# Optimization experiments

Measured on AMD Instinct MI355X. Metric: run time of the kernel, lower is better.

The kernel has to match this reference:

```python
import jax, jax.numpy as jnp
import numpy as np

BN_EPS = 1e-5


def conv3x3(x, w):
    # 3x3 'same' conv, stride 1, no bias (matches nn.Conv2d(k=3, padding=1, bias=False))
    return jax.lax.conv_general_dilated(
        x, w, window_strides=(1, 1), padding='SAME',
        dimension_numbers=('NCHW', 'OIHW', 'NCHW'))


def batchnorm(x, gamma, beta, mean, var):
    # eval-mode BatchNorm2d with running stats
    scale = (gamma / jnp.sqrt(var + BN_EPS))[None, :, None, None]
    return (x - mean[None, :, None, None]) * scale + beta[None, :, None, None]


def setup_inputs() -> dict:
    key = jax.random.key(0)
    ks = jax.random.split(key, 13)
    B, C, H, W = 16, 64, 160, 160
    wshape = (C, C, 3, 3)
    inp = {
        'x': jax.random.normal(ks[0], (B, C, H, W), jnp.float32),
        'w_cv1': jax.random.normal(ks[1], wshape, jnp.float32) * 0.05,
        'g1': jax.random.uniform(ks[2], (C,), jnp.float32, 0.5, 1.5),
        'b1': jax.random.normal(ks[3], (C,), jnp.float32) * 0.1,
        'm1': jax.random.normal(ks[4], (C,), jnp.float32) * 0.1,
        'v1': jax.random.uniform(ks[5], (C,), jnp.float32, 0.5, 1.5),
        'wq': jax.random.normal(ks[6], wshape, jnp.float32) * 0.05,
        'wk': jax.random.normal(ks[7], wshape, jnp.float32) * 0.05,
        'wv': jax.random.normal(ks[8], wshape, jnp.float32) * 0.05,
        'g2': jax.random.uniform(ks[9], (C,), jnp.float32, 0.5, 1.5),
        'b2': jax.random.normal(ks[10], (C,), jnp.float32) * 0.1,
        'm2': jax.random.normal(ks[11], (C,), jnp.float32) * 0.1,
        'v2': jax.random.uniform(ks[12], (C,), jnp.float32, 0.5, 1.5),
    }
    return inp


def reference(x, w_cv1, g1, b1, m1, v1, wq, wk, wv, g2, b2, m2, v2):
    # cv1: Conv -> BN -> SiLU
    y = jax.nn.silu(batchnorm(conv3x3(x, w_cv1), g1, b1, m1, v1))

    # CSA_ConvBlock on y (c_ channels)
    fq = conv3x3(y, wq)   # [B,C,H,W]
    fk = conv3x3(y, wk)
    fv = conv3x3(y, wv)
    H, W = y.shape[2], y.shape[3]

    # Original: f_sim[b,i,j,h1,h2] = sum_w fq[b,i,h1,w]*fk[b,j,h2,w] / sqrt(W);
    # then sum over j, then mean-ish sum over (h1,h2)/H^2 -> f_scores[b,i].
    # Algebraically identical reorder (sum-before-matmul):
    k_sum = fk.sum(axis=(1, 2))                       # [B,W], sum over channels j and rows h2
    scale = 1.0 / (float(W) ** 0.5 * float(H) * float(H))
    f_scores = jnp.einsum('bchw,bw->bc', fq, k_sum) * scale  # [B,C]
    scores = jax.nn.softmax(f_scores, axis=1)[:, :, None, None]

    r = scores * fv + y
    r = jax.nn.relu(batchnorm(r, g2, b2, m2, v2))

    # shortcut: c1 == c2 and shortcut=True
    return x + r
```

## Files before the change

kernel.cpp:

```cpp
#include <hip/hip_runtime.h>
#include <hip/hip_bf16.h>
#include <math.h>

#define NB 16
#define NC 64
#define NH 160
#define NW 160

typedef __attribute__((ext_vector_type(8))) short bf16x8;
typedef __attribute__((ext_vector_type(4))) float f32x4;
typedef __attribute__((ext_vector_type(8))) unsigned short u16x8;
typedef __attribute__((ext_vector_type(4))) unsigned short u16x4;

__device__ __forceinline__ unsigned short f2bf(float v) {
  union { __hip_bfloat16 b; unsigned short u; } cv; cv.b = __float2bfloat16(v); return cv.u;
}
__device__ __forceinline__ float bf2f(unsigned short u) {
  union { unsigned u; float f; } cv; cv.u = ((unsigned)u) << 16; return cv.f;
}

__global__ void pack_w_kernel3(const float* __restrict__ wA, const float* __restrict__ wB,
                               const float* __restrict__ wq, const float* __restrict__ wk,
                               unsigned short* __restrict__ apkA, unsigned short* __restrict__ apkB,
                               float* __restrict__ wqt, float* __restrict__ wkst) {
  int idx = blockIdx.x * 256 + threadIdx.x;
  if (idx < 2 * 36864) {
    const float* w = (idx < 36864) ? wA : wB;
    unsigned short* apk = (idx < 36864) ? apkA : apkB;
    int i = (idx < 36864) ? idx : idx - 36864;
    int j = i & 7, l = (i >> 3) & 63, rest = i >> 9;
    int ks = rest % 18, ct = rest / 18;
    int cih = ks & 1, tap = ks >> 1, kh = tap / 3, kw = tap % 3;
    int co = ct * 16 + (l & 15), ci = cih * 32 + (l >> 4) * 8 + j;
    apk[i] = f2bf(w[(((size_t)co * NC + ci) * 3 + kh) * 3 + kw]);
  } else if (idx < 3 * 36864) {
    int i2 = idx - 2 * 36864;
    int c = i2 & 63, tau = i2 >> 6;
    int i = tau & 63, jj = tau >> 6;
    wqt[i2] = wq[(size_t)c * 576 + i * 9 + jj];
  } else if (idx < 3 * 36864 + 576) {
    int i3 = idx - 3 * 36864;
    int i = i3 & 63, jj = i3 >> 6;
    float s = 0.f;
    for (int cj = 0; cj < NC; ++cj) s += wk[(size_t)cj * 576 + i * 9 + jj];
    wkst[i3] = s;
  }
}

__global__ __launch_bounds__(256) void to_nhwc(const float* __restrict__ x,
                                               unsigned short* __restrict__ xt) {
  __shared__ unsigned short l[64 * 162];
  int bh = blockIdx.x; int b = bh / NH, h = bh % NH;
  for (int i = threadIdx.x; i < 64 * NW; i += 256) {
    int ci = i / NW, w = i % NW;
    l[ci * 162 + w] = f2bf(x[(((size_t)b * NC + ci) * NH + h) * NW + w]);
  }
  __syncthreads();
  unsigned short* o = xt + ((size_t)b * NH + h) * NW * NC;
  for (int i = threadIdx.x; i < NW * 8; i += 256) {
    int w = i >> 3, s = i & 7;
    u16x8 v;
#pragma unroll
    for (int j = 0; j < 8; ++j) v[j] = l[(s * 8 + j) * 162 + w];
    *(u16x8*)&o[w * 64 + s * 8] = v;
  }
}

template<bool FINAL>
__global__ __launch_bounds__(256, FINAL ? 3 : 2) void conv3x3_mfma6(
    const unsigned short* __restrict__ in_nhwc, const unsigned short* __restrict__ apk,
    const float* __restrict__ gg, const float* __restrict__ bbeta,
    const float* __restrict__ mmean, const float* __restrict__ vvar,
    void* __restrict__ outv, const float* __restrict__ scores,
    const float* __restrict__ xres, float* __restrict__ colpart)
{
  __shared__ unsigned short ring[6 * 34 * 64];
  __shared__ unsigned short epi[FINAL ? 8 : 2 * 32 * 72];
  __shared__ f32x4 csv[FINAL ? 1 : 512];

  const int t = threadIdx.x, lane = t & 63, wave = t >> 6;
  const int q = lane >> 4, col = lane & 15;

  int g = blockIdx.x;
  int sw = (g & 7) * 160 + (g >> 3);
  const int b = sw / 80;
  int rem = sw % 80;
  const int h0 = (rem / 5) * 10, w0 = (rem % 5) * 32;

  float scR[4], shR[4], scoR[4];
#pragma unroll
  for (int r = 0; r < 4; ++r) {
    int co = wave * 16 + q * 4 + r;
    float s = gg[co] * rsqrtf(vvar[co] + 1e-5f);
    scR[r] = s; shR[r] = bbeta[co] - mmean[co] * s;
    scoR[r] = FINAL ? scores[b * NC + co] : 0.f;
  }

  bf16x8 wf[18];
#pragma unroll
  for (int ks = 0; ks < 18; ++ks)
    wf[ks] = *(const bf16x8*)&apk[((size_t)(wave * 18 + ks) * 64 + lane) * 8];

  const unsigned short* inb = in_nhwc + (size_t)b * NH * NW * 64;

#define SLOT(R) ((int)((unsigned)((R) + 1) % 6u) * 2176)
#define STG_ISSUE(ROW, V0, V1, A0, A1)                                        \
  { int row_ = (ROW);                                                         \
    bool rowok_ = (unsigned)row_ < (unsigned)NH;                              \
    int slot_ = SLOT(row_);                                                   \
    { int wcc = t >> 3, s8 = t & 7; int wsrc = w0 + wcc - 1;                  \
      A0 = slot_ + wcc * 64 + ((s8 ^ (wcc & 7)) << 3);                        \
      V0 = (u16x8){};                                                         \
      if (rowok_ && (unsigned)wsrc < (unsigned)NW)                            \
        V0 = *(const u16x8*)&inb[((size_t)row_ * NW + wsrc) * 64 + s8 * 8];   \
    }                                                                         \
    if (t < 16) { int c = 256 + t; int wcc = c >> 3, s8 = c & 7;              \
      int wsrc = w0 + wcc - 1;                                                \
      A1 = slot_ + wcc * 64 + ((s8 ^ (wcc & 7)) << 3);                        \
      V1 = (u16x8){};                                                         \
      if (rowok_ && (unsigned)wsrc < (unsigned)NW)                            \
        V1 = *(const u16x8*)&inb[((size_t)row_ * NW + wsrc) * 64 + s8 * 8];   \
    } }
#define STG_COMMIT(V0, V1, A0, A1)                                            \
  *(u16x8*)&ring[A0] = V0;                                                    \
  if (t < 16) *(u16x8*)&ring[A1] = V1;

  if constexpr (!FINAL) {
    csv[t] = (f32x4){0.f, 0.f, 0.f, 0.f};
    csv[t + 256] = (f32x4){0.f, 0.f, 0.f, 0.f};
  }
  for (int rr = -1; rr <= 2; ++rr) {
    u16x8 v0, v1 = {}; int a0, a1 = 0;
    STG_ISSUE(h0 + rr, v0, v1, a0, a1)
    STG_COMMIT(v0, v1, a0, a1)
  }
  __syncthreads();

  for (int wi = 0; wi < 5; ++wi) {
    const int h = h0 + wi * 2;
    u16x8 va0, va1 = {}, vb0, vb1 = {}; int aa0, aa1 = 0, ab0, ab1 = 0;
    const bool doS = (wi < 4);
    if (doS) {
      STG_ISSUE(h + 3, va0, va1, aa0, aa1)
      STG_ISSUE(h + 4, vb0, vb1, ab0, ab1)
    }

    const int sl[4] = { SLOT(h - 1), SLOT(h), SLOT(h + 1), SLOT(h + 2) };
    f32x4 acc[2][2];
#pragma unroll
    for (int o = 0; o < 2; ++o) { acc[o][0] = (f32x4){0,0,0,0}; acc[o][1] = (f32x4){0,0,0,0}; }

#pragma unroll
    for (int ri = 0; ri < 4; ++ri) {
#pragma unroll
      for (int kw = 0; kw < 3; ++kw) {
#pragma unroll
        for (int cih = 0; cih < 2; ++cih) {
          const int wcb = col + kw;
          const int ea = sl[ri] + wcb * 64 + (((cih << 2) + q) ^ (wcb & 7)) * 8;
          const bf16x8* bp = (const bf16x8*)&ring[ea];
          bf16x8 B0 = bp[0], B1 = bp[128];
          if (ri <= 2) {
            const int ks = (ri * 3 + kw) * 2 + cih;
            acc[0][0] = __builtin_amdgcn_mfma_f32_16x16x32_bf16(wf[ks], B0, acc[0][0], 0, 0, 0);
            acc[0][1] = __builtin_amdgcn_mfma_f32_16x16x32_bf16(wf[ks], B1, acc[0][1], 0, 0, 0);
          }
          if (ri >= 1) {
            const int ks = ((ri - 1) * 3 + kw) * 2 + cih;
            acc[1][0] = __builtin_amdgcn_mfma_f32_16x16x32_bf16(wf[ks], B0, acc[1][0], 0, 0, 0);
            acc[1][1] = __builtin_amdgcn_mfma_f32_16x16x32_bf16(wf[ks], B1, acc[1][1], 0, 0, 0);
          }
        }
      }
    }

    if constexpr (!FINAL) {
      f32x4 csadd[2];
      csadd[0] = (f32x4){0,0,0,0}; csadd[1] = (f32x4){0,0,0,0};
#pragma unroll
      for (int o = 0; o < 2; ++o) {
#pragma unroll
        for (int wt = 0; wt < 2; ++wt) {
          u16x4 ev;
#pragma unroll
          for (int r = 0; r < 4; ++r) {
            float z = scR[r] * acc[o][wt][r] + shR[r];
            ev[r] = f2bf(z / (1.f + __expf(-z)));
          }
          *(u16x4*)&epi[((o * 32) + wt * 16 + col) * 72 + wave * 16 + q * 4] = ev;
#pragma unroll
          for (int r = 0; r < 4; ++r) csadd[wt][r] += bf2f(ev[r]);
        }
      }
      { int cc = wave * 4 + q;
        csv[cc * 32 + col]      += csadd[0];
        csv[cc * 32 + 16 + col] += csadd[1]; }
      if (doS) { STG_COMMIT(va0, va1, aa0, aa1) STG_COMMIT(vb0, vb1, ab0, ab1) }
      __syncthreads();
      { int w = t >> 3, s = t & 7;
#pragma unroll
        for (int o = 0; o < 2; ++o) {
          unsigned short* yo = (unsigned short*)outv + (((size_t)b * NH + h + o) * NW + w0) * 64;
          *(u16x8*)&yo[w * 64 + s * 8] = *(const u16x8*)&epi[((o * 32) + w) * 72 + s * 8];
        }
      }
      __syncthreads();
    } else {
      if (doS) { STG_COMMIT(va0, va1, aa0, aa1) STG_COMMIT(vb0, vb1, ab0, ab1) }
      float* outp = (float*)outv;
#pragma unroll
      for (int o = 0; o < 2; ++o) {
        const int rb1 = sl[1 + o];
#pragma unroll
        for (int wt = 0; wt < 2; ++wt) {
          int wcc = wt * 16 + col + 1;
          int gr = (wave * 2 + (q >> 1)) ^ (wcc & 7);
          u16x4 yv = *(const u16x4*)&ring[rb1 + wcc * 64 + gr * 8 + (q & 1) * 4];
#pragma unroll
          for (int r = 0; r < 4; ++r) {
            int co = wave * 16 + q * 4 + r;
            float rv = scoR[r] * acc[o][wt][r] + bf2f(yv[r]);
            float rb_ = scR[r] * rv + shR[r];
            rb_ = fmaxf(rb_, 0.f);
            size_t oi = (((size_t)b * NC + co) * NH + h + o) * NW + w0 + wt * 16 + col;
            outp[oi] = xres[oi] + rb_;
          }
        }
      }
      __syncthreads();
    }
  }

  if constexpr (!FINAL) {
    const int strip = h0 / 10;
    float* pp = colpart + (((size_t)b * 16 + strip) * NW + w0) * 64;
    int w = t >> 3, g0 = t & 7;
    *(f32x4*)&pp[w * 64 + g0 * 4]       = csv[g0 * 32 + w];
    *(f32x4*)&pp[w * 64 + (g0 + 8) * 4] = csv[(g0 + 8) * 32 + w];
  }
#undef STG_ISSUE
#undef STG_COMMIT
#undef SLOT
}

__global__ void colsum2_kernel(const float* __restrict__ part, float* __restrict__ ycol) {
  int id = blockIdx.x * 256 + threadIdx.x;
  if (id >= NB * NW * NC) return;
  int c = id & 63; int bw = id >> 6; int w = bw % NW; int b = bw / NW;
  const float* p = part + (((size_t)b * 16) * NW + w) * 64 + c;
  float s = 0.f;
#pragma unroll
  for (int st = 0; st < 16; ++st) s += p[(size_t)st * NW * 64];
  ycol[id] = s;
}

__device__ __forceinline__ float zval(const float* __restrict__ ycol,
                                      const unsigned short* __restrict__ y,
                                      int b, int i, int kh, int wp) {
  float z = ycol[((size_t)b * NW + wp) * 64 + i];
  if (kh == 0) z -= bf2f(y[(((size_t)b * NH + (NH - 1)) * NW + wp) * 64 + i]);
  if (kh == 2) z -= bf2f(y[(((size_t)b * NH) * NW + wp) * 64 + i]);
  return z;
}

__global__ __launch_bounds__(256) void ks_kernel(
    const float* __restrict__ ycol, const unsigned short* __restrict__ y,
    const float* __restrict__ wkst, float* __restrict__ ks)
{
  int id = blockIdx.x * 4 + (threadIdx.x >> 6);
  int lane = threadIdx.x & 63;
  int b = id / NW, w = id % NW;
  float s = 0.f;
#pragma unroll
  for (int jj = 0; jj < 9; ++jj) {
    int kh = jj / 3, kw = jj % 3;
    int wp = w + kw - 1;
    if ((unsigned)wp < (unsigned)NW)
      s += wkst[jj * 64 + lane] * zval(ycol, y, b, lane, kh, wp);
  }
#pragma unroll
  for (int off = 32; off; off >>= 1) s += __shfl_xor(s, off);
  if (lane == 0) ks[id] = s;
}

__global__ __launch_bounds__(256) void u_kernel(
    const float* __restrict__ ycol, const unsigned short* __restrict__ y,
    const float* __restrict__ ks, float* __restrict__ U)
{
  __shared__ float red[4][64];
  int bid = blockIdx.x;
  int b = bid / 9, jj = bid % 9;
  int kh = jj / 3, kw = jj % 3;
  int i = threadIdx.x & 63, ch = threadIdx.x >> 6;
  float s = 0.f;
  for (int w = ch * 40; w < ch * 40 + 40; ++w) {
    int wp = w + kw - 1;
    if ((unsigned)wp < (unsigned)NW)
      s += zval(ycol, y, b, i, kh, wp) * ks[b * NW + w];
  }
  red[ch][i] = s;
  __syncthreads();
  if (threadIdx.x < 64)
    U[((size_t)b * 9 + jj) * 64 + threadIdx.x] =
        red[0][threadIdx.x] + red[1][threadIdx.x] + red[2][threadIdx.x] + red[3][threadIdx.x];
}

__global__ __launch_bounds__(256) void scores_kernel2(
    const float* __restrict__ wqt, const float* __restrict__ U,
    float* __restrict__ scores)
{
  __shared__ float red[4][64];
  int b = blockIdx.x;
  int c = threadIdx.x & 63, p = threadIdx.x >> 6;
  const float* Ub = U + (size_t)b * 576;
  float s = 0.f;
  for (int tau = p * 144; tau < p * 144 + 144; ++tau)
    s += wqt[(size_t)tau * 64 + c] * Ub[tau];
  red[p][c] = s;
  __syncthreads();
  if (threadIdx.x < 64) {
    const float scale = 1.0f / (sqrtf((float)NW) * (float)NH * (float)NH);
    float f = (red[0][c] + red[1][c] + red[2][c] + red[3][c]) * scale;
    float mx = f;
#pragma unroll
    for (int off = 32; off; off >>= 1) mx = fmaxf(mx, __shfl_xor(mx, off));
    float e = __expf(f - mx);
    float sm = e;
#pragma unroll
    for (int off = 32; off; off >>= 1) sm += __shfl_xor(sm, off);
    scores[b * NC + c] = e / sm;
  }
}

extern "C" void kernel_launch(void* const* d_in, const int* in_sizes, int n_in,
                              void* d_out, int out_size, void* d_ws, size_t ws_size,
                              hipStream_t stream) {
  const float* x  = (const float*)d_in[0];
  const float* w1 = (const float*)d_in[1];
  const float* g1 = (const float*)d_in[2];
  const float* b1 = (const float*)d_in[3];
  const float* m1 = (const float*)d_in[4];
  const float* v1 = (const float*)d_in[5];
  const float* wq = (const float*)d_in[6];
  const float* wk = (const float*)d_in[7];
  const float* wv = (const float*)d_in[8];
  const float* g2 = (const float*)d_in[9];
  const float* b2 = (const float*)d_in[10];
  const float* m2 = (const float*)d_in[11];
  const float* v2 = (const float*)d_in[12];
  float* out = (float*)d_out;

  unsigned short* apk1 = (unsigned short*)d_ws;
  unsigned short* apk2 = apk1 + 36864;
  float* wqt  = (float*)(apk2 + 36864);
  float* wkst = wqt + 36864;
  float* ycol = wkst + 576;
  float* ks   = ycol + NB * NW * NC;
  float* U    = ks + NB * NW;
  float* scr  = U + NB * 576;
  float* part = scr + 1024;
  unsigned short* xt = (unsigned short*)(part + (size_t)NB * 16 * NW * 64);
  unsigned short* y  = xt + (size_t)NB * NH * NW * 64;

  pack_w_kernel3<<<dim3(435), 256, 0, stream>>>(w1, wv, wq, wk, apk1, apk2, wqt, wkst);
  to_nhwc<<<dim3(NB * NH), 256, 0, stream>>>(x, xt);

  conv3x3_mfma6<false><<<dim3(1280), 256, 0, stream>>>(
      xt, apk1, g1, b1, m1, v1, (void*)y, nullptr, nullptr, part);

  colsum2_kernel<<<dim3((NB * NW * NC + 255) / 256), 256, 0, stream>>>(part, ycol);
  ks_kernel<<<dim3(NB * NW / 4), 256, 0, stream>>>(ycol, y, wkst, ks);
  u_kernel<<<dim3(NB * 9), 256, 0, stream>>>(ycol, y, ks, U);
  scores_kernel2<<<dim3(NB), 256, 0, stream>>>(wqt, U, scr);

  conv3x3_mfma6<true><<<dim3(1280), 256, 0, stream>>>(
      y, apk2, g2, b2, m2, v2, (void*)out, scr, x, nullptr);
}
```

Measured before the change: 183.7 us.

## Fuse NCHW-to-NHWC bf16 conversion into first conv and double-buffer epilogue

Drops the separate to_nhwc kernel: the first conv now reads fp32 NCHW input directly, converts it to bf16 and writes the swizzled ring buffer in shared memory. This avoids a full write and re-read of a bf16 NHWC copy of x. The epilogue staging buffer is double-buffered so one barrier per step can be removed, and barriers become a lgkmcnt wait plus s_barrier. The final conv's launch bound drops from 3 to 2 waves per SIMD. The trade-off is strided fp32 channel loads (8 scalar loads per thread across channel planes) in place of 16-byte vector loads, plus more shared memory.

After: 150.4 us (median of 4 runs). -18.2%, faster.

```diff
diff --git a/kernel.cpp b/kernel.cpp
--- a/kernel.cpp
+++ b/kernel.cpp
@@ -18,6 +18,12 @@
 __device__ __forceinline__ float bf2f(unsigned short u) {
   union { unsigned u; float f; } cv; cv.u = ((unsigned)u) << 16; return cv.f;
 }
+
+#define LGKM_BARRIER()                                  \
+  asm volatile("s_waitcnt lgkmcnt(0)" ::: "memory");    \
+  __builtin_amdgcn_sched_barrier(0);                    \
+  __builtin_amdgcn_s_barrier();                         \
+  __builtin_amdgcn_sched_barrier(0);
 
 __global__ void pack_w_kernel3(const float* __restrict__ wA, const float* __restrict__ wB,
                                const float* __restrict__ wq, const float* __restrict__ wk,
@@ -47,35 +53,17 @@
   }
 }
 
-__global__ __launch_bounds__(256) void to_nhwc(const float* __restrict__ x,
-                                               unsigned short* __restrict__ xt) {
-  __shared__ unsigned short l[64 * 162];
-  int bh = blockIdx.x; int b = bh / NH, h = bh % NH;
-  for (int i = threadIdx.x; i < 64 * NW; i += 256) {
-    int ci = i / NW, w = i % NW;
-    l[ci * 162 + w] = f2bf(x[(((size_t)b * NC + ci) * NH + h) * NW + w]);
-  }
-  __syncthreads();
-  unsigned short* o = xt + ((size_t)b * NH + h) * NW * NC;
-  for (int i = threadIdx.x; i < NW * 8; i += 256) {
-    int w = i >> 3, s = i & 7;
-    u16x8 v;
-#pragma unroll
-    for (int j = 0; j < 8; ++j) v[j] = l[(s * 8 + j) * 162 + w];
-    *(u16x8*)&o[w * 64 + s * 8] = v;
-  }
-}
-
 template<bool FINAL>
-__global__ __launch_bounds__(256, FINAL ? 3 : 2) void conv3x3_mfma6(
-    const unsigned short* __restrict__ in_nhwc, const unsigned short* __restrict__ apk,
+__global__ __launch_bounds__(256, 2) void conv3x3_mfma7(
+    const unsigned short* __restrict__ in_nhwc, const float* __restrict__ in_nchw,
+    const unsigned short* __restrict__ apk,
     const float* __restrict__ gg, const float* __restrict__ bbeta,
     const float* __restrict__ mmean, const float* __restrict__ vvar,
     void* __restrict__ outv, const float* __restrict__ scores,
     const float* __restrict__ xres, float* __restrict__ colpart)
 {
   __shared__ unsigned short ring[6 * 34 * 64];
-  __shared__ unsigned short epi[FINAL ? 8 : 2 * 32 * 72];
+  __shared__ unsigned short epi[FINAL ? 8 : 2 * 64 * 72];
   __shared__ f32x4 csv[FINAL ? 1 : 512];
 
   const int t = threadIdx.x, lane = t & 63, wave = t >> 6;
@@ -101,10 +89,12 @@
   for (int ks = 0; ks < 18; ++ks)
     wf[ks] = *(const bf16x8*)&apk[((size_t)(wave * 18 + ks) * 64 + lane) * 8];
 
-  const unsigned short* inb = in_nhwc + (size_t)b * NH * NW * 64;
+  const unsigned short* inb = FINAL ? in_nhwc + (size_t)b * NH * NW * 64 : nullptr;
+  const float* xb = FINAL ? nullptr : in_nchw + (size_t)b * NC * NH * NW;
 
 #define SLOT(R) ((int)((unsigned)((R) + 1) % 6u) * 2176)
-#define STG_ISSUE(ROW, V0, V1, A0, A1)                                        \
+
+#define STGF_ISSUE(ROW, V0, V1, A0, A1)                                       \
   { int row_ = (ROW);                                                         \
     bool rowok_ = (unsigned)row_ < (unsigned)NH;                              \
     int slot_ = SLOT(row_);                                                   \
@@ -121,28 +111,78 @@
       if (rowok_ && (unsigned)wsrc < (unsigned)NW)                            \
         V1 = *(const u16x8*)&inb[((size_t)row_ * NW + wsrc) * 64 + s8 * 8];   \
     } }
-#define STG_COMMIT(V0, V1, A0, A1)                                            \
+#define STGF_COMMIT(V0, V1, A0, A1)                                           \
   *(u16x8*)&ring[A0] = V0;                                                    \
   if (t < 16) *(u16x8*)&ring[A1] = V1;
+
+#define STG1_ISSUE(ROW, F0, F1, A0, A1)                                       \
+  { int row_ = (ROW);                                                         \
+    bool rowok_ = (unsigned)row_ < (unsigned)NH;                              \
+    int slot_ = SLOT(row_);                                                   \
+    { int wcc = t % 34, s8 = t / 34; int wsrc = w0 + wcc - 1;                 \
+      A0 = slot_ + wcc * 64 + ((s8 ^ (wcc & 7)) << 3);                        \
+      bool ok_ = rowok_ && (unsigned)wsrc < (unsigned)NW;                     \
+      if (ok_) {                                                              \
+        const float* xp_ = xb + ((size_t)(s8 * 8) * NH + row_) * NW + wsrc;   \
+        _Pragma("unroll") for (int j_ = 0; j_ < 8; ++j_)                      \
+          F0[j_] = xp_[(size_t)j_ * NH * NW];                                 \
+      } else {                                                                \
+        _Pragma("unroll") for (int j_ = 0; j_ < 8; ++j_) F0[j_] = 0.f;        \
+      }                                                                       \
+    }                                                                         \
+    if (t < 16) { int wcc = 18 + t; int wsrc = w0 + wcc - 1;                  \
+      A1 = slot_ + wcc * 64 + ((7 ^ (wcc & 7)) << 3);                         \
+      bool ok_ = rowok_ && (unsigned)wsrc < (unsigned)NW;                     \
+      if (ok_) {                                                              \
+        const float* xp_ = xb + ((size_t)56 * NH + row_) * NW + wsrc;         \
+        _Pragma("unroll") for (int j_ = 0; j_ < 8; ++j_)                      \
+          F1[j_] = xp_[(size_t)j_ * NH * NW];                                 \
+      } else {                                                                \
+        _Pragma("unroll") for (int j_ = 0; j_ < 8; ++j_) F1[j_] = 0.f;        \
+      }                                                                       \
+    } }
+#define STG1_COMMIT(F0, F1, A0, A1)                                           \
+  { u16x8 pv_;                                                                \
+    _Pragma("unroll") for (int j_ = 0; j_ < 8; ++j_) pv_[j_] = f2bf(F0[j_]);  \
+    *(u16x8*)&ring[A0] = pv_; }                                               \
+  if (t < 16) { u16x8 pv_;                                                    \
+    _Pragma("unroll") for (int j_ = 0; j_ < 8; ++j_) pv_[j_] = f2bf(F1[j_]);  \
+    *(u16x8*)&ring[A1] = pv_; }
 
   if constexpr (!FINAL) {
     csv[t] = (f32x4){0.f, 0.f, 0.f, 0.f};
     csv[t + 256] = (f32x4){0.f, 0.f, 0.f, 0.f};
   }
-  for (int rr = -1; rr <= 2; ++rr) {
-    u16x8 v0, v1 = {}; int a0, a1 = 0;
-    STG_ISSUE(h0 + rr, v0, v1, a0, a1)
-    STG_COMMIT(v0, v1, a0, a1)
-  }
-  __syncthreads();
+
+  if constexpr (FINAL) {
+    for (int rr = -1; rr <= 2; ++rr) {
+      u16x8 v0, v1 = {}; int a0, a1 = 0;
+      STGF_ISSUE(h0 + rr, v0, v1, a0, a1)
+      STGF_COMMIT(v0, v1, a0, a1)
+    }
+  } else {
+    for (int rr = -1; rr <= 2; ++rr) {
+      float f0[8], f1[8]; int a0, a1 = 0;
+      STG1_ISSUE(h0 + rr, f0, f1, a0, a1)
+      STG1_COMMIT(f0, f1, a0, a1)
+    }
+  }
+  LGKM_BARRIER()
 
   for (int wi = 0; wi < 5; ++wi) {
     const int h = h0 + wi * 2;
+    const bool doS = (wi < 4);
+
     u16x8 va0, va1 = {}, vb0, vb1 = {}; int aa0, aa1 = 0, ab0, ab1 = 0;
-    const bool doS = (wi < 4);
+    float fa0[8], fa1[8], fb0[8], fb1[8];
     if (doS) {
-      STG_ISSUE(h + 3, va0, va1, aa0, aa1)
-      STG_ISSUE(h + 4, vb0, vb1, ab0, ab1)
+      if constexpr (FINAL) {
+        STGF_ISSUE(h + 3, va0, va1, aa0, aa1)
+        STGF_ISSUE(h + 4, vb0, vb1, ab0, ab1)
+      } else {
+        STG1_ISSUE(h + 3, fa0, fa1, aa0, aa1)
+        STG1_ISSUE(h + 4, fb0, fb1, ab0, ab1)
+      }
     }
 
     const int sl[4] = { SLOT(h - 1), SLOT(h), SLOT(h + 1), SLOT(h + 2) };
@@ -175,6 +215,7 @@
     }
 
     if constexpr (!FINAL) {
+      const int buf = (wi & 1) * 4608;
       f32x4 csadd[2];
       csadd[0] = (f32x4){0,0,0,0}; csadd[1] = (f32x4){0,0,0,0};
 #pragma unroll
@@ -187,7 +228,7 @@
             float z = scR[r] * acc[o][wt][r] + shR[r];
             ev[r] = f2bf(z / (1.f + __expf(-z)));
           }
-          *(u16x4*)&epi[((o * 32) + wt * 16 + col) * 72 + wave * 16 + q * 4] = ev;
+          *(u16x4*)&epi[buf + ((o * 32) + wt * 16 + col) * 72 + wave * 16 + q * 4] = ev;
 #pragma unroll
           for (int r = 0; r < 4; ++r) csadd[wt][r] += bf2f(ev[r]);
         }
@@ -195,18 +236,17 @@
       { int cc = wave * 4 + q;
         csv[cc * 32 + col]      += csadd[0];
         csv[cc * 32 + 16 + col] += csadd[1]; }
-      if (doS) { STG_COMMIT(va0, va1, aa0, aa1) STG_COMMIT(vb0, vb1, ab0, ab1) }
-      __syncthreads();
+      if (doS) { STG1_COMMIT(fa0, fa1, aa0, aa1) STG1_COMMIT(fb0, fb1, ab0, ab1) }
+      LGKM_BARRIER()
       { int w = t >> 3, s = t & 7;
 #pragma unroll
         for (int o = 0; o < 2; ++o) {
           unsigned short* yo = (unsigned short*)outv + (((size_t)b * NH + h + o) * NW + w0) * 64;
-          *(u16x8*)&yo[w * 64 + s * 8] = *(const u16x8*)&epi[((o * 32) + w) * 72 + s * 8];
+          *(u16x8*)&yo[w * 64 + s * 8] = *(const u16x8*)&epi[buf + ((o * 32) + w) * 72 + s * 8];
         }
       }
-      __syncthreads();
     } else {
-      if (doS) { STG_COMMIT(va0, va1, aa0, aa1) STG_COMMIT(vb0, vb1, ab0, ab1) }
+      if (doS) { STGF_COMMIT(va0, va1, aa0, aa1) STGF_COMMIT(vb0, vb1, ab0, ab1) }
       float* outp = (float*)outv;
 #pragma unroll
       for (int o = 0; o < 2; ++o) {
@@ -227,7 +267,7 @@
           }
         }
       }
-      __syncthreads();
+      LGKM_BARRIER()
     }
   }
 
@@ -238,8 +278,10 @@
     *(f32x4*)&pp[w * 64 + g0 * 4]       = csv[g0 * 32 + w];
     *(f32x4*)&pp[w * 64 + (g0 + 8) * 4] = csv[(g0 + 8) * 32 + w];
   }
-#undef STG_ISSUE
-#undef STG_COMMIT
+#undef STG1_ISSUE
+#undef STG1_COMMIT
+#undef STGF_ISSUE
+#undef STGF_COMMIT
 #undef SLOT
 }
 
@@ -359,20 +401,18 @@
   float* U    = ks + NB * NW;
   float* scr  = U + NB * 576;
   float* part = scr + 1024;
-  unsigned short* xt = (unsigned short*)(part + (size_t)NB * 16 * NW * 64);
-  unsigned short* y  = xt + (size_t)NB * NH * NW * 64;
+  unsigned short* y = (unsigned short*)(part + (size_t)NB * 16 * NW * 64);
 
   pack_w_kernel3<<<dim3(435), 256, 0, stream>>>(w1, wv, wq, wk, apk1, apk2, wqt, wkst);
-  to_nhwc<<<dim3(NB * NH), 256, 0, stream>>>(x, xt);
-
-  conv3x3_mfma6<false><<<dim3(1280), 256, 0, stream>>>(
-      xt, apk1, g1, b1, m1, v1, (void*)y, nullptr, nullptr, part);
+
+  conv3x3_mfma7<false><<<dim3(1280), 256, 0, stream>>>(
+      nullptr, x, apk1, g1, b1, m1, v1, (void*)y, nullptr, nullptr, part);
 
   colsum2_kernel<<<dim3((NB * NW * NC + 255) / 256), 256, 0, stream>>>(part, ycol);
   ks_kernel<<<dim3(NB * NW / 4), 256, 0, stream>>>(ycol, y, wkst, ks);
   u_kernel<<<dim3(NB * 9), 256, 0, stream>>>(ycol, y, ks, U);
   scores_kernel2<<<dim3(NB), 256, 0, stream>>>(wqt, U, scr);
 
-  conv3x3_mfma6<true><<<dim3(1280), 256, 0, stream>>>(
-      y, apk2, g2, b2, m2, v2, (void*)out, scr, x, nullptr);
-}
+  conv3x3_mfma7<true><<<dim3(1280), 256, 0, stream>>>(
+      y, nullptr, apk2, g2, b2, m2, v2, (void*)out, scr, x, nullptr);
+}
```
